# Performance work log

Measured on AMD Instinct MI355X. Metric: run time of the kernel, lower is better.

The kernel has to match this reference:

```python
import jax, jax.numpy as jnp
import numpy as np

NEG_SLOPE = 0.2  # PyG GATConv default negative_slope
EPS = 1e-16     # PyG softmax denominator epsilon


def gat_layer(x, src, dst, W, att_src, att_dst, bias, N):
    """PyG-style GATConv: gather -> leaky-relu score -> segment softmax -> scatter-add.
    x: [N, F_in], W: [F_in, H*C], att_src/att_dst: [H, C], bias: [H*C].
    src/dst: [E] edge endpoints (messages flow src -> dst), self-loops included.
    """
    H, C = att_src.shape
    h = (x @ W).reshape(N, H, C)                       # [N, H, C]
    a_s = jnp.sum(h * att_src, axis=-1)                # [N, H]
    a_d = jnp.sum(h * att_dst, axis=-1)                # [N, H]
    e = a_s[src] + a_d[dst]                            # [E, H]
    e = jnp.where(e > 0, e, NEG_SLOPE * e)             # leaky relu
    m = jax.ops.segment_max(e, dst, num_segments=N)    # [N, H] (self-loops ensure every node hit)
    p = jnp.exp(e - m[dst])                            # [E, H]
    s = jax.ops.segment_sum(p, dst, num_segments=N)    # [N, H]
    alpha = p / (s[dst] + EPS)                         # [E, H]
    out = jax.ops.segment_sum(alpha[:, :, None] * h[src], dst, num_segments=N)  # [N, H, C]
    return out.reshape(N, H * C) + bias


def setup_inputs() -> dict:
    key = jax.random.key(0)
    ks = jax.random.split(key, 12)
    N, E = 100000, 1600000
    x = jax.random.normal(ks[0], (N, 1), dtype=jnp.float32)
    edge_index = jax.random.randint(ks[1], (2, E), 0, N, dtype=jnp.int32)
    sc = 0.1
    # conv1: in=1, heads=4, out=8
    W1 = jax.random.normal(ks[2], (1, 32), dtype=jnp.float32) * sc
    att_src1 = jax.random.normal(ks[3], (4, 8), dtype=jnp.float32) * sc
    att_dst1 = jax.random.normal(ks[4], (4, 8), dtype=jnp.float32) * sc
    bias1 = jnp.zeros((32,), dtype=jnp.float32)
    # conv2: in=32, heads=8, out=8
    W2 = jax.random.normal(ks[5], (32, 64), dtype=jnp.float32) * sc
    att_src2 = jax.random.normal(ks[6], (8, 8), dtype=jnp.float32) * sc
    att_dst2 = jax.random.normal(ks[7], (8, 8), dtype=jnp.float32) * sc
    bias2 = jnp.zeros((64,), dtype=jnp.float32)
    # fc2: 64 -> 1
    fc_w = jax.random.normal(ks[8], (64, 1), dtype=jnp.float32) * sc
    fc_b = jnp.zeros((1,), dtype=jnp.float32)
    return {"x": x, "edge_index": edge_index,
            "W1": W1, "att_src1": att_src1, "att_dst1": att_dst1, "bias1": bias1,
            "W2": W2, "att_src2": att_src2, "att_dst2": att_dst2, "bias2": bias2,
            "fc_w": fc_w, "fc_b": fc_b}


def reference(x, edge_index, W1, att_src1, att_dst1, bias1,
              W2, att_src2, att_dst2, bias2, fc_w, fc_b):
    N = x.shape[0]
    loop = jnp.arange(N, dtype=edge_index.dtype)       # add_self_loops=True (PyG default)
    src = jnp.concatenate([edge_index[0], loop])
    dst = jnp.concatenate([edge_index[1], loop])
    h = jax.nn.elu(gat_layer(x, src, dst, W1, att_src1, att_dst1, bias1, N))
    h = jax.nn.elu(gat_layer(h, src, dst, W2, att_src2, att_dst2, bias2, N))
    return h @ fc_w + fc_b                             # [N, 1]
```

## Files before the change

### kernel.cpp

```cpp
#include <hip/hip_runtime.h>
#include <hip/hip_fp16.h>
#include <cmath>

#define TPB 256
#define NSLOPE 0.2f
#define SEPS 1e-16f

#define BSH 7
#define BNODES 128
#define NBMAX 1024
#define NCHUNK 512
#define SCTPB 1024
#define STAGE 2816
#define MAXDEG 96

__device__ __forceinline__ float lrelu(float v) { return v > 0.f ? v : NSLOPE * v; }
__device__ __forceinline__ float elu1(float v)  { return v > 0.f ? v : expm1f(v); }
__device__ __forceinline__ float elu1f(float v) { return v > 0.f ? v : __expf(v) - 1.f; }

__global__ void k_prep(const float* __restrict__ W1, const float* __restrict__ as1,
                       const float* __restrict__ ad1, float* __restrict__ SD,
                       unsigned* __restrict__ bucketCursor, int NB, unsigned cap) {
    int t = threadIdx.x;
    for (int i = t; i < NB; i += blockDim.x) bucketCursor[(size_t)i * 16] = (unsigned)i * cap;
    if (t < 8) {
        int h = t & 3;
        const float* att = (t >= 4) ? ad1 : as1;
        float acc = 0.f;
        #pragma unroll
        for (int c = 0; c < 8; ++c) acc += W1[h*8+c] * att[h*8+c];
        SD[t] = acc;
    }
}

__global__ void k_bscatter(const int* __restrict__ srcI, const int* __restrict__ dstI,
                           int E, int N, int NB, int chunk,
                           unsigned* __restrict__ bucketCursor, int* __restrict__ pk) {
    __shared__ int cnt[NBMAX];
    __shared__ unsigned base[NBMAX];
    for (int i = threadIdx.x; i < NB; i += blockDim.x) cnt[i] = 0;
    __syncthreads();
    int ET = E + N;
    int beg = blockIdx.x * chunk;
    int end = min(beg + chunk, ET);
    for (int e = beg + threadIdx.x; e < end; e += blockDim.x) {
        int d = (e < E) ? dstI[e] : (e - E);
        atomicAdd(&cnt[d >> BSH], 1);
    }
    __syncthreads();
    for (int i = threadIdx.x; i < NB; i += blockDim.x) {
        int c = cnt[i];
        base[i] = c ? atomicAdd(&bucketCursor[(size_t)i * 16], (unsigned)c) : 0u;
        cnt[i] = 0;
    }
    __syncthreads();
    for (int e = beg + threadIdx.x; e < end; e += blockDim.x) {
        int s, d;
        if (e < E) { s = srcI[e]; d = dstI[e]; } else { s = d = e - E; }
        int b = d >> BSH;
        int r = atomicAdd(&cnt[b], 1);
        pk[base[b] + r] = (s << BSH) | (d & (BNODES - 1));
    }
}

__global__ void k_sort(const int* __restrict__ pk, const unsigned* __restrict__ bucketCursor,
                       unsigned cap, int N,
                       unsigned* __restrict__ offsets, int* __restrict__ sortedSrc) {
    __shared__ int stage[STAGE];
    __shared__ int sorted[STAGE];
    __shared__ int cnt[BNODES];
    __shared__ int offl[BNODES];
    int b = blockIdx.x, t = threadIdx.x;
    unsigned rbeg = (unsigned)b * cap;
    int m = (int)(bucketCursor[(size_t)b * 16] - rbeg);
    if (t < BNODES) cnt[t] = 0;
    if (m <= STAGE) {
        for (int i = t; i < m; i += TPB) stage[i] = pk[rbeg + i];
        __syncthreads();
        for (int i = t; i < m; i += TPB) atomicAdd(&cnt[stage[i] & (BNODES - 1)], 1);
        __syncthreads();
        int v = (t < BNODES) ? cnt[t] : 0;
        if (t < BNODES) offl[t] = v;
        __syncthreads();
        for (int off = 1; off < BNODES; off <<= 1) {
            int u = (t >= off && t < BNODES) ? offl[t - off] : 0;
            __syncthreads();
            if (t < BNODES) offl[t] += u;
            __syncthreads();
        }
        if (t < BNODES) {
            int ex = offl[t] - v;
            int d = (b << BSH) + t;
            if (d < N) offsets[d] = ((rbeg + (unsigned)ex) << 10) | (unsigned)v;
            cnt[t] = 0;
            offl[t] = ex;
        }
        __syncthreads();
        for (int i = t; i < m; i += TPB) {
            int p = stage[i];
            int dl = p & (BNODES - 1);
            int r = atomicAdd(&cnt[dl], 1);
            sorted[offl[dl] + r] = p >> BSH;
        }
        __syncthreads();
        for (int i = t; i < m; i += TPB) sortedSrc[rbeg + i] = sorted[i];
    } else {
        __syncthreads();
        for (int i = t; i < m; i += TPB) atomicAdd(&cnt[pk[rbeg + i] & (BNODES - 1)], 1);
        __syncthreads();
        int v = (t < BNODES) ? cnt[t] : 0;
        if (t < BNODES) offl[t] = v;
        __syncthreads();
        for (int off = 1; off < BNODES; off <<= 1) {
            int u = (t >= off && t < BNODES) ? offl[t - off] : 0;
            __syncthreads();
            if (t < BNODES) offl[t] += u;
            __syncthreads();
        }
        if (t < BNODES) {
            int ex = offl[t] - v;
            int d = (b << BSH) + t;
            if (d < N) offsets[d] = ((rbeg + (unsigned)ex) << 10) | (unsigned)v;
            cnt[t] = 0;
            offl[t] = ex;
        }
        __syncthreads();
        for (int i = t; i < m; i += TPB) {
            int p = pk[rbeg + i];
            int dl = p & (BNODES - 1);
            int r = atomicAdd(&cnt[dl], 1);
            sortedSrc[rbeg + (unsigned)(offl[dl] + r)] = p >> BSH;
        }
    }
}

__global__ void k_l1h2(const unsigned* __restrict__ offsets, const int* __restrict__ sortedSrc,
                       const float* __restrict__ x, const float* __restrict__ SD,
                       const float* __restrict__ W1, const float* __restrict__ b1,
                       const float* __restrict__ W2, const float* __restrict__ attS,
                       const float* __restrict__ attD, int N,
                       __half* __restrict__ h2h, float* __restrict__ aS, float* __restrict__ aD) {
    __shared__ float lds1[BNODES][36];
    int t = threadIdx.x;
    int base = blockIdx.x << BSH;
    int n = t >> 1, half = t & 1;
    int d = base + n;
    bool active = (d < N);
    float s0 = 0.f, s1 = 0.f, s2 = 0.f, s3 = 0.f;
    float g0 = 0.f, g1 = 0.f, g2 = 0.f, g3 = 0.f;
    if (active) {
        unsigned u = offsets[d];
        unsigned beg = u >> 10;
        int deg = (int)(u & 1023u);
        float xd = x[d];
        float S0 = SD[0], S1 = SD[1], S2 = SD[2], S3 = SD[3];
        float D0 = xd*SD[4], D1 = xd*SD[5], D2 = xd*SD[6], D3 = xd*SD[7];
        int d2 = (deg + 1) >> 1;
        unsigned i = beg + (half ? (unsigned)d2 : 0u);
        int rem = half ? (deg - d2) : d2;
        for (; rem >= 2; rem -= 2, i += 2) {
            int a0 = sortedSrc[i], a1 = sortedSrc[i+1];
            float x0 = x[a0], x1 = x[a1];
            float p;
            p = __expf(lrelu(x0*S0 + D0)); s0 += p; g0 += p * x0;
            p = __expf(lrelu(x0*S1 + D1)); s1 += p; g1 += p * x0;
            p = __expf(lrelu(x0*S2 + D2)); s2 += p; g2 += p * x0;
            p = __expf(lrelu(x0*S3 + D3)); s3 += p; g3 += p * x0;
            p = __expf(lrelu(x1*S0 + D0)); s0 += p; g0 += p * x1;
            p = __expf(lrelu(x1*S1 + D1)); s1 += p; g1 += p * x1;
            p = __expf(lrelu(x1*S2 + D2)); s2 += p; g2 += p * x1;
            p = __expf(lrelu(x1*S3 + D3)); s3 += p; g3 += p * x1;
        }
        if (rem > 0) {
            float xs = x[sortedSrc[i]];
            float p;
            p = __expf(lrelu(xs*S0 + D0)); s0 += p; g0 += p * xs;
            p = __expf(lrelu(xs*S1 + D1)); s1 += p; g1 += p * xs;
            p = __expf(lrelu(xs*S2 + D2)); s2 += p; g2 += p * xs;
            p = __expf(lrelu(xs*S3 + D3)); s3 += p; g3 += p * xs;
        }
    }
    s0 += __shfl_xor(s0, 1); s1 += __shfl_xor(s1, 1);
    s2 += __shfl_xor(s2, 1); s3 += __shfl_xor(s3, 1);
    g0 += __shfl_xor(g0, 1); g1 += __shfl_xor(g1, 1);
    g2 += __shfl_xor(g2, 1); g3 += __shfl_xor(g3, 1);
    if (active) {
        float gg[4];
        gg[0] = g0 / (s0 + SEPS); gg[1] = g1 / (s1 + SEPS);
        gg[2] = g2 / (s2 + SEPS); gg[3] = g3 / (s3 + SEPS);
        int h0 = half * 2;
        #pragma unroll
        for (int hh = 0; hh < 2; ++hh)
            #pragma unroll
            for (int cc = 0; cc < 8; ++cc)
                lds1[n][(h0+hh)*8+cc] = elu1(gg[h0+hh] * W1[(h0+hh)*8+cc] + b1[(h0+hh)*8+cc]);
    }
    __syncthreads();
    int lane = t & 63;
    int sub = t >> 6;
    float w2r[32];
    #pragma unroll
    for (int k = 0; k < 32; ++k) w2r[k] = W2[k*64 + lane];
    float attSl = attS[lane], attDl = attD[lane];
    int nCnt = min(BNODES, N - base);
    for (int nn = sub; nn < nCnt; nn += 4) {
        const float4* row4 = (const float4*)lds1[nn];
        float acc = 0.f;
        #pragma unroll
        for (int k4 = 0; k4 < 8; ++k4) {
            float4 rv = row4[k4];
            acc += rv.x*w2r[4*k4] + rv.y*w2r[4*k4+1] + rv.z*w2r[4*k4+2] + rv.w*w2r[4*k4+3];
        }
        int node = base + nn;
        h2h[(size_t)node*64 + lane] = __float2half(acc);
        float ps = acc * attSl;
        float pd = acc * attDl;
        #pragma unroll
        for (int m = 1; m < 8; m <<= 1) {
            ps += __shfl_xor(ps, m);
            pd += __shfl_xor(pd, m);
        }
        int hh = lane >> 3, cc = lane & 7;
        if (cc == 0) aS[(size_t)node*8 + hh] = ps;
        if (cc == 1) aD[(size_t)node*8 + hh] = pd;
    }
}

__global__ void k_agg(const unsigned* __restrict__ offsets, const int* __restrict__ ss,
                      const float* __restrict__ aS, const float* __restrict__ aD,
                      const __half* __restrict__ h2h, const float* __restrict__ b2,
                      const float* __restrict__ fcw, const float* __restrict__ fcb,
                      float* __restrict__ out, int N) {
    __shared__ float pl[4][MAXDEG * 8];
    __shared__ int   sl[4][MAXDEG];
    int lane = threadIdx.x & 63;
    int w = threadIdx.x >> 6;
    int d = blockIdx.x * 4 + w;
    if (d >= N) return;
    unsigned u = offsets[d];
    unsigned beg = u >> 10;
    int deg = (int)(u & 1023u);
    int lH   = lane & 31;
    int half = lane >> 5;
    int hh   = lH >> 2;
    float sum = 0.f, ax = 0.f, ay = 0.f;
    if (deg <= MAXDEG) {
        for (int j = lane; j < deg; j += 64) sl[w][j] = ss[beg + j];
        float adp = aD[(size_t)d*8 + (lane & 7)];
        int tot = deg * 8;
        for (int base = 0; base < tot; base += 64) {
            int idx = base + lane;
            if (idx < tot) {
                int s = sl[w][idx >> 3];
                pl[w][idx] = __expf(lrelu(aS[(size_t)s*8 + (lane & 7)] + adp));
            }
        }
        int e = 0;
        for (; e + 8 <= deg; e += 8) {
            int e0 = e + half, e1 = e + 2 + half, e2 = e + 4 + half, e3 = e + 6 + half;
            int s0 = sl[w][e0], s1 = sl[w][e1], s2 = sl[w][e2], s3 = sl[w][e3];
            float p0 = pl[w][e0*8 + hh], p1 = pl[w][e1*8 + hh];
            float p2 = pl[w][e2*8 + hh], p3 = pl[w][e3*8 + hh];
            float2 g0 = __half22float2(*(const __half2*)(h2h + (size_t)s0*64 + 2*lH));
            float2 g1 = __half22float2(*(const __half2*)(h2h + (size_t)s1*64 + 2*lH));
            float2 g2 = __half22float2(*(const __half2*)(h2h + (size_t)s2*64 + 2*lH));
            float2 g3 = __half22float2(*(const __half2*)(h2h + (size_t)s3*64 + 2*lH));
            ax += p0*g0.x + p1*g1.x + p2*g2.x + p3*g3.x;
            ay += p0*g0.y + p1*g1.y + p2*g2.y + p3*g3.y;
            sum += (p0 + p1) + (p2 + p3);
        }
        for (; e + 2 <= deg; e += 2) {
            int e0 = e + half;
            int s0 = sl[w][e0];
            float p0 = pl[w][e0*8 + hh];
            float2 g0 = __half22float2(*(const __half2*)(h2h + (size_t)s0*64 + 2*lH));
            ax += p0*g0.x; ay += p0*g0.y; sum += p0;
        }
        if (e < deg) {
            int s0 = sl[w][e];
            float p0 = (half == 0) ? pl[w][e*8 + hh] : 0.f;
            float2 g0 = __half22float2(*(const __half2*)(h2h + (size_t)s0*64 + 2*lH));
            ax += p0*g0.x; ay += p0*g0.y; sum += p0;
        }
    } else {
        float adh = aD[(size_t)d*8 + hh];
        for (int e = half; e < deg; e += 2) {
            int s = ss[beg + e];
            float p = __expf(lrelu(aS[(size_t)s*8 + hh] + adh));
            float2 g = __half22float2(*(const __half2*)(h2h + (size_t)s*64 + 2*lH));
            ax += p*g.x; ay += p*g.y; sum += p;
        }
    }
    ax  += __shfl_xor(ax, 32);
    ay  += __shfl_xor(ay, 32);
    sum += __shfl_xor(sum, 32);
    float inv = 1.f / (sum + SEPS);
    float tt = elu1f(ax*inv + b2[2*lH]) * fcw[2*lH]
             + elu1f(ay*inv + b2[2*lH+1]) * fcw[2*lH+1];
    #pragma unroll
    for (int m = 16; m; m >>= 1) tt += __shfl_xor(tt, m);
    if (lane == 0) out[d] = tt + fcb[0];
}

extern "C" void kernel_launch(void* const* d_in, const int* in_sizes, int n_in,
                              void* d_out, int out_size, void* d_ws, size_t ws_size,
                              hipStream_t stream) {
    const float* x    = (const float*)d_in[0];
    const int*   ei   = (const int*)  d_in[1];
    const float* W1   = (const float*)d_in[2];
    const float* as1  = (const float*)d_in[3];
    const float* ad1  = (const float*)d_in[4];
    const float* b1   = (const float*)d_in[5];
    const float* W2   = (const float*)d_in[6];
    const float* attS2= (const float*)d_in[7];
    const float* attD2= (const float*)d_in[8];
    const float* b2   = (const float*)d_in[9];
    const float* fcw  = (const float*)d_in[10];
    const float* fcb  = (const float*)d_in[11];
    float* out = (float*)d_out;

    int N = in_sizes[0];
    int E = in_sizes[1] / 2;
    int ET = E + N;
    int NB = (N + BNODES - 1) / BNODES;
    unsigned cap = (unsigned)((ET + NB - 1) / NB + 512);
    cap = (cap + 3u) & ~3u;
    size_t padded = (size_t)NB * cap;

    const int* srcI = ei;
    const int* dstI = ei + E;

    float* ws = (float*)d_ws;
    size_t off = 0;
    float*    SD           = ws + off; off += 16;
    unsigned* bucketCursor = (unsigned*)(ws + off); off += (size_t)NBMAX * 16;
    unsigned* offsets      = (unsigned*)(ws + off); off += (size_t)N + 16;
    int*      pk           = (int*)(ws + off); off += padded;
    int*      sortedSrc    = (int*)(ws + off); off += padded;
    float*    aS2          = ws + off; off += (size_t)N * 8;
    float*    aD2          = ws + off; off += (size_t)N * 8;
    __half*   h2h          = (__half*)(ws + off); off += (size_t)N * 32;

    k_prep<<<1, 1024, 0, stream>>>(W1, as1, ad1, SD, bucketCursor, NB, cap);

    int chunk = (ET + NCHUNK - 1) / NCHUNK;
    k_bscatter<<<NCHUNK, SCTPB, 0, stream>>>(srcI, dstI, E, N, NB, chunk, bucketCursor, pk);
    k_sort    <<<NB, TPB, 0, stream>>>(pk, bucketCursor, cap, N, offsets, sortedSrc);
    k_l1h2    <<<NB, TPB, 0, stream>>>(offsets, sortedSrc, x, SD, W1, b1, W2, attS2, attD2,
                                       N, h2h, aS2, aD2);
    k_agg     <<<(N + 3) / 4, TPB, 0, stream>>>(offsets, sortedSrc, aS2, aD2, h2h,
                                                b2, fcw, fcb, out, N);
}
```

Baseline: 224.2 us.

## Fuse bucket sort with layer-1 aggregation and stage scatter writes in LDS

Merges the per-bucket sort kernel and the layer-1 attention/projection kernel into one kernel. The fused kernel reads neighbor lists and per-node degree/offset straight from LDS, so it skips one launch and a global re-read of sortedSrc and offsets. The bucket scatter kernel now sorts each chunk's edges by bucket in shared memory before writing them out, so the global writes to pk are more contiguous. In exchange it uses more LDS per block, which may reduce occupancy, and adds a 1024-entry block scan.

```diff
diff --git a/kernel.cpp b/kernel.cpp
--- a/kernel.cpp
+++ b/kernel.cpp
@@ -11,6 +11,7 @@
 #define NBMAX 1024
 #define NCHUNK 512
 #define SCTPB 1024
+#define SCSTAGE 3360
 #define STAGE 2816
 #define MAXDEG 96
 
@@ -38,64 +39,108 @@
                            unsigned* __restrict__ bucketCursor, int* __restrict__ pk) {
     __shared__ int cnt[NBMAX];
     __shared__ unsigned base[NBMAX];
-    for (int i = threadIdx.x; i < NB; i += blockDim.x) cnt[i] = 0;
-    __syncthreads();
+    __shared__ int offl[NBMAX];
+    __shared__ int rval[SCSTAGE];
+    __shared__ unsigned short rbkt[SCSTAGE];
+    int t = threadIdx.x;
     int ET = E + N;
     int beg = blockIdx.x * chunk;
     int end = min(beg + chunk, ET);
-    for (int e = beg + threadIdx.x; e < end; e += blockDim.x) {
+    int m = end - beg;
+    for (int i = t; i < NBMAX; i += blockDim.x) cnt[i] = 0;
+    __syncthreads();
+    for (int e = beg + t; e < end; e += blockDim.x) {
         int d = (e < E) ? dstI[e] : (e - E);
         atomicAdd(&cnt[d >> BSH], 1);
     }
     __syncthreads();
-    for (int i = threadIdx.x; i < NB; i += blockDim.x) {
-        int c = cnt[i];
-        base[i] = c ? atomicAdd(&bucketCursor[(size_t)i * 16], (unsigned)c) : 0u;
-        cnt[i] = 0;
-    }
-    __syncthreads();
-    for (int e = beg + threadIdx.x; e < end; e += blockDim.x) {
-        int s, d;
-        if (e < E) { s = srcI[e]; d = dstI[e]; } else { s = d = e - E; }
-        int b = d >> BSH;
-        int r = atomicAdd(&cnt[b], 1);
-        pk[base[b] + r] = (s << BSH) | (d & (BNODES - 1));
-    }
-}
-
-__global__ void k_sort(const int* __restrict__ pk, const unsigned* __restrict__ bucketCursor,
-                       unsigned cap, int N,
-                       unsigned* __restrict__ offsets, int* __restrict__ sortedSrc) {
+    int v = (t < NBMAX) ? cnt[t] : 0;
+    if (t < NBMAX) base[t] = (unsigned)v;
+    __syncthreads();
+    for (int off = 1; off < NBMAX; off <<= 1) {
+        unsigned u = (t >= off && t < NBMAX) ? base[t - off] : 0u;
+        __syncthreads();
+        if (t < NBMAX) base[t] += u;
+        __syncthreads();
+    }
+    if (t < NBMAX) offl[t] = (int)base[t] - v;
+    __syncthreads();
+    if (t < NB) {
+        base[t] = v ? atomicAdd(&bucketCursor[(size_t)t * 16], (unsigned)v) : 0u;
+        cnt[t] = 0;
+    }
+    __syncthreads();
+    if (m <= SCSTAGE) {
+        for (int e = beg + t; e < end; e += blockDim.x) {
+            int s, d;
+            if (e < E) { s = srcI[e]; d = dstI[e]; } else { s = d = e - E; }
+            int b = d >> BSH;
+            int r = atomicAdd(&cnt[b], 1);
+            int slot = offl[b] + r;
+            rval[slot] = (s << BSH) | (d & (BNODES - 1));
+            rbkt[slot] = (unsigned short)b;
+        }
+        __syncthreads();
+        for (int slot = t; slot < m; slot += blockDim.x) {
+            int b = rbkt[slot];
+            pk[base[b] + (unsigned)(slot - offl[b])] = rval[slot];
+        }
+    } else {
+        for (int e = beg + t; e < end; e += blockDim.x) {
+            int s, d;
+            if (e < E) { s = srcI[e]; d = dstI[e]; } else { s = d = e - E; }
+            int b = d >> BSH;
+            int r = atomicAdd(&cnt[b], 1);
+            pk[base[b] + (unsigned)r] = (s << BSH) | (d & (BNODES - 1));
+        }
+    }
+}
+
+__global__ void k_mega(const int* __restrict__ pk, const unsigned* __restrict__ bucketCursor,
+                       unsigned cap,
+                       const float* __restrict__ x, const float* __restrict__ SD,
+                       const float* __restrict__ W1, const float* __restrict__ b1,
+                       const float* __restrict__ W2, const float* __restrict__ attS,
+                       const float* __restrict__ attD, int N,
+                       unsigned* __restrict__ offsets, int* __restrict__ sortedSrc,
+                       __half* __restrict__ h2h, float* __restrict__ aS, float* __restrict__ aD) {
     __shared__ int stage[STAGE];
     __shared__ int sorted[STAGE];
     __shared__ int cnt[BNODES];
     __shared__ int offl[BNODES];
+    __shared__ float lds1[BNODES][36];
     int b = blockIdx.x, t = threadIdx.x;
     unsigned rbeg = (unsigned)b * cap;
     int m = (int)(bucketCursor[(size_t)b * 16] - rbeg);
+    bool inLds = (m <= STAGE);
     if (t < BNODES) cnt[t] = 0;
-    if (m <= STAGE) {
+    __syncthreads();
+    if (inLds) {
         for (int i = t; i < m; i += TPB) stage[i] = pk[rbeg + i];
         __syncthreads();
         for (int i = t; i < m; i += TPB) atomicAdd(&cnt[stage[i] & (BNODES - 1)], 1);
-        __syncthreads();
-        int v = (t < BNODES) ? cnt[t] : 0;
-        if (t < BNODES) offl[t] = v;
-        __syncthreads();
-        for (int off = 1; off < BNODES; off <<= 1) {
-            int u = (t >= off && t < BNODES) ? offl[t - off] : 0;
-            __syncthreads();
-            if (t < BNODES) offl[t] += u;
-            __syncthreads();
-        }
-        if (t < BNODES) {
-            int ex = offl[t] - v;
-            int d = (b << BSH) + t;
-            if (d < N) offsets[d] = ((rbeg + (unsigned)ex) << 10) | (unsigned)v;
-            cnt[t] = 0;
-            offl[t] = ex;
-        }
-        __syncthreads();
+    } else {
+        for (int i = t; i < m; i += TPB) atomicAdd(&cnt[pk[rbeg + i] & (BNODES - 1)], 1);
+    }
+    __syncthreads();
+    int v = (t < BNODES) ? cnt[t] : 0;
+    if (t < BNODES) offl[t] = v;
+    __syncthreads();
+    for (int off = 1; off < BNODES; off <<= 1) {
+        int u = (t >= off && t < BNODES) ? offl[t - off] : 0;
+        __syncthreads();
+        if (t < BNODES) offl[t] += u;
+        __syncthreads();
+    }
+    if (t < BNODES) {
+        int ex = offl[t] - v;
+        int d = (b << BSH) + t;
+        if (d < N) offsets[d] = ((rbeg + (unsigned)ex) << 10) | (unsigned)v;
+        cnt[t] = 0;
+        offl[t] = ex;
+    }
+    __syncthreads();
+    if (inLds) {
         for (int i = t; i < m; i += TPB) {
             int p = stage[i];
             int dl = p & (BNODES - 1);
@@ -105,61 +150,34 @@
         __syncthreads();
         for (int i = t; i < m; i += TPB) sortedSrc[rbeg + i] = sorted[i];
     } else {
-        __syncthreads();
-        for (int i = t; i < m; i += TPB) atomicAdd(&cnt[pk[rbeg + i] & (BNODES - 1)], 1);
-        __syncthreads();
-        int v = (t < BNODES) ? cnt[t] : 0;
-        if (t < BNODES) offl[t] = v;
-        __syncthreads();
-        for (int off = 1; off < BNODES; off <<= 1) {
-            int u = (t >= off && t < BNODES) ? offl[t - off] : 0;
-            __syncthreads();
-            if (t < BNODES) offl[t] += u;
-            __syncthreads();
-        }
-        if (t < BNODES) {
-            int ex = offl[t] - v;
-            int d = (b << BSH) + t;
-            if (d < N) offsets[d] = ((rbeg + (unsigned)ex) << 10) | (unsigned)v;
-            cnt[t] = 0;
-            offl[t] = ex;
-        }
-        __syncthreads();
         for (int i = t; i < m; i += TPB) {
             int p = pk[rbeg + i];
             int dl = p & (BNODES - 1);
             int r = atomicAdd(&cnt[dl], 1);
             sortedSrc[rbeg + (unsigned)(offl[dl] + r)] = p >> BSH;
         }
-    }
-}
-
-__global__ void k_l1h2(const unsigned* __restrict__ offsets, const int* __restrict__ sortedSrc,
-                       const float* __restrict__ x, const float* __restrict__ SD,
-                       const float* __restrict__ W1, const float* __restrict__ b1,
-                       const float* __restrict__ W2, const float* __restrict__ attS,
-                       const float* __restrict__ attD, int N,
-                       __half* __restrict__ h2h, float* __restrict__ aS, float* __restrict__ aD) {
-    __shared__ float lds1[BNODES][36];
-    int t = threadIdx.x;
-    int base = blockIdx.x << BSH;
+        __syncthreads();
+    }
+    __syncthreads();
     int n = t >> 1, half = t & 1;
-    int d = base + n;
-    bool active = (d < N);
+    int base2 = b << BSH;
+    int d2 = base2 + n;
+    bool active = (d2 < N);
     float s0 = 0.f, s1 = 0.f, s2 = 0.f, s3 = 0.f;
     float g0 = 0.f, g1 = 0.f, g2 = 0.f, g3 = 0.f;
     if (active) {
-        unsigned u = offsets[d];
-        unsigned beg = u >> 10;
-        int deg = (int)(u & 1023u);
-        float xd = x[d];
+        int deg = cnt[n];
+        int lbeg = offl[n];
+        float xd = x[d2];
         float S0 = SD[0], S1 = SD[1], S2 = SD[2], S3 = SD[3];
         float D0 = xd*SD[4], D1 = xd*SD[5], D2 = xd*SD[6], D3 = xd*SD[7];
-        int d2 = (deg + 1) >> 1;
-        unsigned i = beg + (half ? (unsigned)d2 : 0u);
-        int rem = half ? (deg - d2) : d2;
+        int dh = (deg + 1) >> 1;
+        int i0 = lbeg + (half ? dh : 0);
+        int rem = half ? (deg - dh) : dh;
+        int i = i0;
         for (; rem >= 2; rem -= 2, i += 2) {
-            int a0 = sortedSrc[i], a1 = sortedSrc[i+1];
+            int a0 = inLds ? sorted[i]   : sortedSrc[rbeg + i];
+            int a1 = inLds ? sorted[i+1] : sortedSrc[rbeg + i + 1];
             float x0 = x[a0], x1 = x[a1];
             float p;
             p = __expf(lrelu(x0*S0 + D0)); s0 += p; g0 += p * x0;
@@ -172,7 +190,8 @@
             p = __expf(lrelu(x1*S3 + D3)); s3 += p; g3 += p * x1;
         }
         if (rem > 0) {
-            float xs = x[sortedSrc[i]];
+            int a0 = inLds ? sorted[i] : sortedSrc[rbeg + i];
+            float xs = x[a0];
             float p;
             p = __expf(lrelu(xs*S0 + D0)); s0 += p; g0 += p * xs;
             p = __expf(lrelu(xs*S1 + D1)); s1 += p; g1 += p * xs;
@@ -202,7 +221,7 @@
     #pragma unroll
     for (int k = 0; k < 32; ++k) w2r[k] = W2[k*64 + lane];
     float attSl = attS[lane], attDl = attD[lane];
-    int nCnt = min(BNODES, N - base);
+    int nCnt = min(BNODES, N - base2);
     for (int nn = sub; nn < nCnt; nn += 4) {
         const float4* row4 = (const float4*)lds1[nn];
         float acc = 0.f;
@@ -211,14 +230,14 @@
             float4 rv = row4[k4];
             acc += rv.x*w2r[4*k4] + rv.y*w2r[4*k4+1] + rv.z*w2r[4*k4+2] + rv.w*w2r[4*k4+3];
         }
-        int node = base + nn;
+        int node = base2 + nn;
         h2h[(size_t)node*64 + lane] = __float2half(acc);
         float ps = acc * attSl;
         float pd = acc * attDl;
         #pragma unroll
-        for (int m = 1; m < 8; m <<= 1) {
-            ps += __shfl_xor(ps, m);
-            pd += __shfl_xor(pd, m);
+        for (int mm = 1; mm < 8; mm <<= 1) {
+            ps += __shfl_xor(ps, mm);
+            pd += __shfl_xor(pd, mm);
         }
         int hh = lane >> 3, cc = lane & 7;
         if (cc == 0) aS[(size_t)node*8 + hh] = ps;
@@ -345,9 +364,8 @@
 
     int chunk = (ET + NCHUNK - 1) / NCHUNK;
     k_bscatter<<<NCHUNK, SCTPB, 0, stream>>>(srcI, dstI, E, N, NB, chunk, bucketCursor, pk);
-    k_sort    <<<NB, TPB, 0, stream>>>(pk, bucketCursor, cap, N, offsets, sortedSrc);
-    k_l1h2    <<<NB, TPB, 0, stream>>>(offsets, sortedSrc, x, SD, W1, b1, W2, attS2, attD2,
-                                       N, h2h, aS2, aD2);
+    k_mega    <<<NB, TPB, 0, stream>>>(pk, bucketCursor, cap, x, SD, W1, b1, W2, attS2, attD2,
+                                       N, offsets, sortedSrc, h2h, aS2, aD2);
     k_agg     <<<(N + 3) / 4, TPB, 0, stream>>>(offsets, sortedSrc, aS2, aD2, h2h,
                                                 b2, fcw, fcb, out, N);
 }
```

Result: slower. 229.0 us (+2.1%).

## Fuse bucket sort with layer-1 aggregation and W2 projection into one kernel

Applied to the files above, without the earlier changes.

Merges the per-bucket counting sort with the first GAT layer. Layer-1 softmax sums are accumulated with shared-memory float atomics during the counting pass, so the second pass over sorted edges and the separate kernel launch go away. The edge-list reread and the offsets round trip are replaced by LDS atomic contention, and the atomics make the summation order nondeterministic. The final aggregation is also split into two launches over node halves, which looks neutral or like an experiment.

```diff
diff --git a/kernel.cpp b/kernel.cpp
--- a/kernel.cpp
+++ b/kernel.cpp
@@ -63,39 +63,74 @@
     }
 }
 
-__global__ void k_sort(const int* __restrict__ pk, const unsigned* __restrict__ bucketCursor,
-                       unsigned cap, int N,
-                       unsigned* __restrict__ offsets, int* __restrict__ sortedSrc) {
+__global__ void k_mega(const int* __restrict__ pk, const unsigned* __restrict__ bucketCursor,
+                       unsigned cap,
+                       const float* __restrict__ x, const float* __restrict__ SD,
+                       const float* __restrict__ W1, const float* __restrict__ b1,
+                       const float* __restrict__ W2, const float* __restrict__ attS,
+                       const float* __restrict__ attD, int N,
+                       unsigned* __restrict__ offsets, int* __restrict__ sortedSrc,
+                       __half* __restrict__ h2h, float* __restrict__ aS, float* __restrict__ aD) {
     __shared__ int stage[STAGE];
     __shared__ int sorted[STAGE];
     __shared__ int cnt[BNODES];
     __shared__ int offl[BNODES];
+    __shared__ float sAcc[BNODES * 4];
+    __shared__ float gAcc[BNODES * 4];
+    __shared__ float xloc[BNODES];
+    __shared__ float lds1[BNODES][36];
     int b = blockIdx.x, t = threadIdx.x;
     unsigned rbeg = (unsigned)b * cap;
     int m = (int)(bucketCursor[(size_t)b * 16] - rbeg);
-    if (t < BNODES) cnt[t] = 0;
-    if (m <= STAGE) {
+    bool inLds = (m <= STAGE);
+    int base2 = b << BSH;
+    if (t < BNODES) {
+        cnt[t] = 0;
+        int d = base2 + t;
+        xloc[t] = (d < N) ? x[d] : 0.f;
+    }
+    for (int i = t; i < BNODES * 4; i += TPB) { sAcc[i] = 0.f; gAcc[i] = 0.f; }
+    if (inLds)
         for (int i = t; i < m; i += TPB) stage[i] = pk[rbeg + i];
+    __syncthreads();
+    float S0 = SD[0], S1 = SD[1], S2 = SD[2], S3 = SD[3];
+    float D4 = SD[4], D5 = SD[5], D6 = SD[6], D7 = SD[7];
+    for (int i = t; i < m; i += TPB) {
+        int p = inLds ? stage[i] : pk[rbeg + i];
+        int dl = p & (BNODES - 1);
+        int s  = p >> BSH;
+        atomicAdd(&cnt[dl], 1);
+        float xs = x[s];
+        float xd = xloc[dl];
+        float p0 = __expf(lrelu(xs*S0 + xd*D4));
+        float p1 = __expf(lrelu(xs*S1 + xd*D5));
+        float p2 = __expf(lrelu(xs*S2 + xd*D6));
+        float p3 = __expf(lrelu(xs*S3 + xd*D7));
+        int a = dl * 4;
+        atomicAdd(&sAcc[a+0], p0); atomicAdd(&gAcc[a+0], p0 * xs);
+        atomicAdd(&sAcc[a+1], p1); atomicAdd(&gAcc[a+1], p1 * xs);
+        atomicAdd(&sAcc[a+2], p2); atomicAdd(&gAcc[a+2], p2 * xs);
+        atomicAdd(&sAcc[a+3], p3); atomicAdd(&gAcc[a+3], p3 * xs);
+    }
+    __syncthreads();
+    int v = (t < BNODES) ? cnt[t] : 0;
+    if (t < BNODES) offl[t] = v;
+    __syncthreads();
+    for (int off = 1; off < BNODES; off <<= 1) {
+        int u = (t >= off && t < BNODES) ? offl[t - off] : 0;
         __syncthreads();
-        for (int i = t; i < m; i += TPB) atomicAdd(&cnt[stage[i] & (BNODES - 1)], 1);
+        if (t < BNODES) offl[t] += u;
         __syncthreads();
-        int v = (t < BNODES) ? cnt[t] : 0;
-        if (t < BNODES) offl[t] = v;
-        __syncthreads();
-        for (int off = 1; off < BNODES; off <<= 1) {
-            int u = (t >= off && t < BNODES) ? offl[t - off] : 0;
-            __syncthreads();
-            if (t < BNODES) offl[t] += u;
-            __syncthreads();
-        }
-        if (t < BNODES) {
-            int ex = offl[t] - v;
-            int d = (b << BSH) + t;
-            if (d < N) offsets[d] = ((rbeg + (unsigned)ex) << 10) | (unsigned)v;
-            cnt[t] = 0;
-            offl[t] = ex;
-        }
-        __syncthreads();
+    }
+    if (t < BNODES) {
+        int ex = offl[t] - v;
+        int d = base2 + t;
+        if (d < N) offsets[d] = ((rbeg + (unsigned)ex) << 10) | (unsigned)v;
+        cnt[t] = 0;
+        offl[t] = ex;
+    }
+    __syncthreads();
+    if (inLds) {
         for (int i = t; i < m; i += TPB) {
             int p = stage[i];
             int dl = p & (BNODES - 1);
@@ -105,95 +140,28 @@
         __syncthreads();
         for (int i = t; i < m; i += TPB) sortedSrc[rbeg + i] = sorted[i];
     } else {
-        __syncthreads();
-        for (int i = t; i < m; i += TPB) atomicAdd(&cnt[pk[rbeg + i] & (BNODES - 1)], 1);
-        __syncthreads();
-        int v = (t < BNODES) ? cnt[t] : 0;
-        if (t < BNODES) offl[t] = v;
-        __syncthreads();
-        for (int off = 1; off < BNODES; off <<= 1) {
-            int u = (t >= off && t < BNODES) ? offl[t - off] : 0;
-            __syncthreads();
-            if (t < BNODES) offl[t] += u;
-            __syncthreads();
-        }
-        if (t < BNODES) {
-            int ex = offl[t] - v;
-            int d = (b << BSH) + t;
-            if (d < N) offsets[d] = ((rbeg + (unsigned)ex) << 10) | (unsigned)v;
-            cnt[t] = 0;
-            offl[t] = ex;
-        }
-        __syncthreads();
         for (int i = t; i < m; i += TPB) {
             int p = pk[rbeg + i];
             int dl = p & (BNODES - 1);
             int r = atomicAdd(&cnt[dl], 1);
             sortedSrc[rbeg + (unsigned)(offl[dl] + r)] = p >> BSH;
         }
-    }
-}
-
-__global__ void k_l1h2(const unsigned* __restrict__ offsets, const int* __restrict__ sortedSrc,
-                       const float* __restrict__ x, const float* __restrict__ SD,
-                       const float* __restrict__ W1, const float* __restrict__ b1,
-                       const float* __restrict__ W2, const float* __restrict__ attS,
-                       const float* __restrict__ attD, int N,
-                       __half* __restrict__ h2h, float* __restrict__ aS, float* __restrict__ aD) {
-    __shared__ float lds1[BNODES][36];
-    int t = threadIdx.x;
-    int base = blockIdx.x << BSH;
-    int n = t >> 1, half = t & 1;
-    int d = base + n;
-    bool active = (d < N);
-    float s0 = 0.f, s1 = 0.f, s2 = 0.f, s3 = 0.f;
-    float g0 = 0.f, g1 = 0.f, g2 = 0.f, g3 = 0.f;
-    if (active) {
-        unsigned u = offsets[d];
-        unsigned beg = u >> 10;
-        int deg = (int)(u & 1023u);
-        float xd = x[d];
-        float S0 = SD[0], S1 = SD[1], S2 = SD[2], S3 = SD[3];
-        float D0 = xd*SD[4], D1 = xd*SD[5], D2 = xd*SD[6], D3 = xd*SD[7];
-        int d2 = (deg + 1) >> 1;
-        unsigned i = beg + (half ? (unsigned)d2 : 0u);
-        int rem = half ? (deg - d2) : d2;
-        for (; rem >= 2; rem -= 2, i += 2) {
-            int a0 = sortedSrc[i], a1 = sortedSrc[i+1];
-            float x0 = x[a0], x1 = x[a1];
-            float p;
-            p = __expf(lrelu(x0*S0 + D0)); s0 += p; g0 += p * x0;
-            p = __expf(lrelu(x0*S1 + D1)); s1 += p; g1 += p * x0;
-            p = __expf(lrelu(x0*S2 + D2)); s2 += p; g2 += p * x0;
-            p = __expf(lrelu(x0*S3 + D3)); s3 += p; g3 += p * x0;
-            p = __expf(lrelu(x1*S0 + D0)); s0 += p; g0 += p * x1;
-            p = __expf(lrelu(x1*S1 + D1)); s1 += p; g1 += p * x1;
-            p = __expf(lrelu(x1*S2 + D2)); s2 += p; g2 += p * x1;
-            p = __expf(lrelu(x1*S3 + D3)); s3 += p; g3 += p * x1;
-        }
-        if (rem > 0) {
-            float xs = x[sortedSrc[i]];
-            float p;
-            p = __expf(lrelu(xs*S0 + D0)); s0 += p; g0 += p * xs;
-            p = __expf(lrelu(xs*S1 + D1)); s1 += p; g1 += p * xs;
-            p = __expf(lrelu(xs*S2 + D2)); s2 += p; g2 += p * xs;
-            p = __expf(lrelu(xs*S3 + D3)); s3 += p; g3 += p * xs;
-        }
-    }
-    s0 += __shfl_xor(s0, 1); s1 += __shfl_xor(s1, 1);
-    s2 += __shfl_xor(s2, 1); s3 += __shfl_xor(s3, 1);
-    g0 += __shfl_xor(g0, 1); g1 += __shfl_xor(g1, 1);
-    g2 += __shfl_xor(g2, 1); g3 += __shfl_xor(g3, 1);
-    if (active) {
-        float gg[4];
-        gg[0] = g0 / (s0 + SEPS); gg[1] = g1 / (s1 + SEPS);
-        gg[2] = g2 / (s2 + SEPS); gg[3] = g3 / (s3 + SEPS);
-        int h0 = half * 2;
-        #pragma unroll
-        for (int hh = 0; hh < 2; ++hh)
+        __syncthreads();
+    }
+    {
+        int n = t >> 1, half = t & 1;
+        int d = base2 + n;
+        if (d < N) {
+            int h0 = half * 2;
             #pragma unroll
-            for (int cc = 0; cc < 8; ++cc)
-                lds1[n][(h0+hh)*8+cc] = elu1(gg[h0+hh] * W1[(h0+hh)*8+cc] + b1[(h0+hh)*8+cc]);
+            for (int hh = 0; hh < 2; ++hh) {
+                int h = h0 + hh;
+                float gg = gAcc[n*4+h] / (sAcc[n*4+h] + SEPS);
+                #pragma unroll
+                for (int cc = 0; cc < 8; ++cc)
+                    lds1[n][h*8+cc] = elu1(gg * W1[h*8+cc] + b1[h*8+cc]);
+            }
+        }
     }
     __syncthreads();
     int lane = t & 63;
@@ -202,7 +170,7 @@
     #pragma unroll
     for (int k = 0; k < 32; ++k) w2r[k] = W2[k*64 + lane];
     float attSl = attS[lane], attDl = attD[lane];
-    int nCnt = min(BNODES, N - base);
+    int nCnt = min(BNODES, N - base2);
     for (int nn = sub; nn < nCnt; nn += 4) {
         const float4* row4 = (const float4*)lds1[nn];
         float acc = 0.f;
@@ -211,14 +179,14 @@
             float4 rv = row4[k4];
             acc += rv.x*w2r[4*k4] + rv.y*w2r[4*k4+1] + rv.z*w2r[4*k4+2] + rv.w*w2r[4*k4+3];
         }
-        int node = base + nn;
+        int node = base2 + nn;
         h2h[(size_t)node*64 + lane] = __float2half(acc);
         float ps = acc * attSl;
         float pd = acc * attDl;
         #pragma unroll
-        for (int m = 1; m < 8; m <<= 1) {
-            ps += __shfl_xor(ps, m);
-            pd += __shfl_xor(pd, m);
+        for (int mm = 1; mm < 8; mm <<= 1) {
+            ps += __shfl_xor(ps, mm);
+            pd += __shfl_xor(pd, mm);
         }
         int hh = lane >> 3, cc = lane & 7;
         if (cc == 0) aS[(size_t)node*8 + hh] = ps;
@@ -230,13 +198,13 @@
                       const float* __restrict__ aS, const float* __restrict__ aD,
                       const __half* __restrict__ h2h, const float* __restrict__ b2,
                       const float* __restrict__ fcw, const float* __restrict__ fcb,
-                      float* __restrict__ out, int N) {
+                      float* __restrict__ out, int d0, int dEnd) {
     __shared__ float pl[4][MAXDEG * 8];
     __shared__ int   sl[4][MAXDEG];
     int lane = threadIdx.x & 63;
     int w = threadIdx.x >> 6;
-    int d = blockIdx.x * 4 + w;
-    if (d >= N) return;
+    int d = d0 + blockIdx.x * 4 + w;
+    if (d >= dEnd) return;
     unsigned u = offsets[d];
     unsigned beg = u >> 10;
     int deg = (int)(u & 1023u);
@@ -345,9 +313,11 @@
 
     int chunk = (ET + NCHUNK - 1) / NCHUNK;
     k_bscatter<<<NCHUNK, SCTPB, 0, stream>>>(srcI, dstI, E, N, NB, chunk, bucketCursor, pk);
-    k_sort    <<<NB, TPB, 0, stream>>>(pk, bucketCursor, cap, N, offsets, sortedSrc);
-    k_l1h2    <<<NB, TPB, 0, stream>>>(offsets, sortedSrc, x, SD, W1, b1, W2, attS2, attD2,
-                                       N, h2h, aS2, aD2);
-    k_agg     <<<(N + 3) / 4, TPB, 0, stream>>>(offsets, sortedSrc, aS2, aD2, h2h,
-                                                b2, fcw, fcb, out, N);
-}
+    k_mega    <<<NB, TPB, 0, stream>>>(pk, bucketCursor, cap, x, SD, W1, b1, W2, attS2, attD2,
+                                       N, offsets, sortedSrc, h2h, aS2, aD2);
+    int half = ((N + 7) / 8) * 4;
+    k_agg     <<<(half + 3) / 4, TPB, 0, stream>>>(offsets, sortedSrc, aS2, aD2, h2h,
+                                                   b2, fcw, fcb, out, 0, half);
+    k_agg     <<<(N - half + 3) / 4, TPB, 0, stream>>>(offsets, sortedSrc, aS2, aD2, h2h,
+                                                       b2, fcw, fcb, out, half, N);
+}
```

Measured after the change: 313.9 us. +40.0%, slower.

## Stage bucket scatter through shared memory and split aggregation launch in two

Applied to the files above, without the earlier changes.

The bucket scatter kernel now computes a block-local prefix sum over bucket counts, writes packed edges into a shared-memory staging array grouped by bucket, and then writes them to global memory so that writes to each bucket are contiguous. This targets the scattered, uncoalesced global writes of the original per-edge scatter, at the cost of an extra shared-memory pass, a 1024-step scan with many barriers, and higher shared-memory use per block. The aggregation kernel is also launched as two halves over node ranges, which adds a launch but has no clear overlap benefit on a single stream.

```diff
diff --git a/kernel.cpp b/kernel.cpp
--- a/kernel.cpp
+++ b/kernel.cpp
@@ -11,6 +11,7 @@
 #define NBMAX 1024
 #define NCHUNK 512
 #define SCTPB 1024
+#define SCSTAGE 3360
 #define STAGE 2816
 #define MAXDEG 96
 
@@ -38,28 +39,60 @@
                            unsigned* __restrict__ bucketCursor, int* __restrict__ pk) {
     __shared__ int cnt[NBMAX];
     __shared__ unsigned base[NBMAX];
-    for (int i = threadIdx.x; i < NB; i += blockDim.x) cnt[i] = 0;
-    __syncthreads();
+    __shared__ int offl[NBMAX];
+    __shared__ int rval[SCSTAGE];
+    __shared__ unsigned short rbkt[SCSTAGE];
+    int t = threadIdx.x;
     int ET = E + N;
     int beg = blockIdx.x * chunk;
     int end = min(beg + chunk, ET);
-    for (int e = beg + threadIdx.x; e < end; e += blockDim.x) {
+    int m = end - beg;
+    for (int i = t; i < NBMAX; i += blockDim.x) cnt[i] = 0;
+    __syncthreads();
+    for (int e = beg + t; e < end; e += blockDim.x) {
         int d = (e < E) ? dstI[e] : (e - E);
         atomicAdd(&cnt[d >> BSH], 1);
     }
     __syncthreads();
-    for (int i = threadIdx.x; i < NB; i += blockDim.x) {
-        int c = cnt[i];
-        base[i] = c ? atomicAdd(&bucketCursor[(size_t)i * 16], (unsigned)c) : 0u;
-        cnt[i] = 0;
-    }
-    __syncthreads();
-    for (int e = beg + threadIdx.x; e < end; e += blockDim.x) {
-        int s, d;
-        if (e < E) { s = srcI[e]; d = dstI[e]; } else { s = d = e - E; }
-        int b = d >> BSH;
-        int r = atomicAdd(&cnt[b], 1);
-        pk[base[b] + r] = (s << BSH) | (d & (BNODES - 1));
+    int v = (t < NBMAX) ? cnt[t] : 0;
+    if (t < NBMAX) base[t] = (unsigned)v;
+    __syncthreads();
+    for (int off = 1; off < NBMAX; off <<= 1) {
+        unsigned u = (t >= off && t < NBMAX) ? base[t - off] : 0u;
+        __syncthreads();
+        if (t < NBMAX) base[t] += u;
+        __syncthreads();
+    }
+    if (t < NBMAX) offl[t] = (int)base[t] - v;
+    __syncthreads();
+    if (t < NB) {
+        base[t] = v ? atomicAdd(&bucketCursor[(size_t)t * 16], (unsigned)v) : 0u;
+        cnt[t] = 0;
+    }
+    __syncthreads();
+    if (m <= SCSTAGE) {
+        for (int e = beg + t; e < end; e += blockDim.x) {
+            int s, d;
+            if (e < E) { s = srcI[e]; d = dstI[e]; } else { s = d = e - E; }
+            int b = d >> BSH;
+            int r = atomicAdd(&cnt[b], 1);
+            int slot = offl[b] + r;
+            rval[slot] = (s << BSH) | (d & (BNODES - 1));
+            rbkt[slot] = (unsigned short)b;
+        }
+        __syncthreads();
+        for (int slot = t; slot < m; slot += blockDim.x) {
+            int b = rbkt[slot];
+            pk[base[b] + (unsigned)(slot - offl[b])] = rval[slot];
+        }
+    } else {
+        for (int e = beg + t; e < end; e += blockDim.x) {
+            int s, d;
+            if (e < E) { s = srcI[e]; d = dstI[e]; } else { s = d = e - E; }
+            int b = d >> BSH;
+            int r = atomicAdd(&cnt[b], 1);
+            pk[base[b] + (unsigned)r] = (s << BSH) | (d & (BNODES - 1));
+        }
     }
 }
 
@@ -230,13 +263,13 @@
                       const float* __restrict__ aS, const float* __restrict__ aD,
                       const __half* __restrict__ h2h, const float* __restrict__ b2,
                       const float* __restrict__ fcw, const float* __restrict__ fcb,
-                      float* __restrict__ out, int N) {
+                      float* __restrict__ out, int d0, int dEnd) {
     __shared__ float pl[4][MAXDEG * 8];
     __shared__ int   sl[4][MAXDEG];
     int lane = threadIdx.x & 63;
     int w = threadIdx.x >> 6;
-    int d = blockIdx.x * 4 + w;
-    if (d >= N) return;
+    int d = d0 + blockIdx.x * 4 + w;
+    if (d >= dEnd) return;
     unsigned u = offsets[d];
     unsigned beg = u >> 10;
     int deg = (int)(u & 1023u);
@@ -348,6 +381,9 @@
     k_sort    <<<NB, TPB, 0, stream>>>(pk, bucketCursor, cap, N, offsets, sortedSrc);
     k_l1h2    <<<NB, TPB, 0, stream>>>(offsets, sortedSrc, x, SD, W1, b1, W2, attS2, attD2,
                                        N, h2h, aS2, aD2);
-    k_agg     <<<(N + 3) / 4, TPB, 0, stream>>>(offsets, sortedSrc, aS2, aD2, h2h,
-                                                b2, fcw, fcb, out, N);
-}
+    int half = ((N + 7) / 8) * 4;
+    k_agg     <<<(half + 3) / 4, TPB, 0, stream>>>(offsets, sortedSrc, aS2, aD2, h2h,
+                                                   b2, fcw, fcb, out, 0, half);
+    k_agg     <<<(N - half + 3) / 4, TPB, 0, stream>>>(offsets, sortedSrc, aS2, aD2, h2h,
+                                                       b2, fcw, fcb, out, half, N);
+}
```

Measured after the change: 226.4 us. About the same (+1.0%).
